# Kernel optimization log

Measured on AMD Instinct MI355X. Metric: run time of the kernel, lower is better.

Reference implementation:

```python
import jax, jax.numpy as jnp
import numpy as np

DIM = 768
NUM_HEADS = 12
HEAD_DIM = DIM // NUM_HEADS
SCALE = HEAD_DIM ** -0.5


def setup_inputs() -> dict:
    key = jax.random.key(0)
    k1, k2, k3, k4 = jax.random.split(key, 4)
    x = jax.random.normal(k1, (4, 2048, DIM), dtype=jnp.float32)
    # Linear weights stored as [in, out] (torch stores [out, in]; math identical)
    w_qkv = jax.random.normal(k2, (DIM, 3 * DIM), dtype=jnp.float32) * (DIM ** -0.5)
    w_proj = jax.random.normal(k3, (DIM, DIM), dtype=jnp.float32) * (DIM ** -0.5)
    b_proj = jax.random.normal(k4, (DIM,), dtype=jnp.float32) * 0.02
    return {"x": x, "w_qkv": w_qkv, "w_proj": w_proj, "b_proj": b_proj}


def reference(x, w_qkv, w_proj, b_proj):
    b, n, d = x.shape
    qkv = x @ w_qkv  # [b, n, 3*d]
    # '(qkv h d)' layout: leading split is qkv, then heads, then head_dim
    qkv = qkv.reshape(b, n, 3, NUM_HEADS, HEAD_DIM).transpose(2, 0, 3, 1, 4)
    q, k, v = qkv[0], qkv[1], qkv[2]  # each [b, h, n, hd]
    alpha = jnp.einsum('bhqd,bhkd->bhqk', q, k) * SCALE  # [b, h, n, n]
    attn = jax.nn.softmax(alpha, axis=-1)
    out = jnp.einsum('bhqk,bhkd->bhqd', attn, v)  # [b, h, n, hd]
    out = out.transpose(0, 2, 1, 3).reshape(b, n, d)  # b n (h d)
    return out @ w_proj + b_proj
```

## Files before the change

### kernel.cpp

```cpp
#include <hip/hip_runtime.h>
#include <hip/hip_bf16.h>


typedef short s16x8 __attribute__((ext_vector_type(8)));
typedef short s16x4 __attribute__((ext_vector_type(4)));
typedef float f32x4 __attribute__((ext_vector_type(4)));
typedef float f32x16 __attribute__((ext_vector_type(16)));
typedef unsigned int u32;
typedef unsigned int u32x2 __attribute__((ext_vector_type(2)));
typedef unsigned int u32x4 __attribute__((ext_vector_type(4)));

#define NHEADS 12
#define HDIM   64
#define SEQ    2048
#define BATCH  4
#define DMODEL 768
#define MTOT   (BATCH*SEQ)
#define K3     (3*DMODEL)
#define QSCALE 0.18033688f

#define CAST_BLOCKS ((MTOT * DMODEL / 4) / 256)
#define TQ_BLOCKS   ((K3 / 64) * (DMODEL / 64))
#define TP_BLOCKS   ((DMODEL / 64) * (DMODEL / 64))

__device__ __forceinline__ short f2bf(float f) {
  return __builtin_bit_cast(short, __float2bfloat16(f));
}
__device__ __forceinline__ u32 pack2bf_rh(float lo, float hi) {
  u32 a = __builtin_bit_cast(u32, lo) + 0x8000u;
  u32 b = __builtin_bit_cast(u32, hi) + 0x8000u;
  return __builtin_amdgcn_perm(b, a, 0x07060302u);
}
__device__ __forceinline__ u32 pack2bf_tr(float lo, float hi) {
  return __builtin_amdgcn_perm(__builtin_bit_cast(u32, hi),
                               __builtin_bit_cast(u32, lo), 0x07060302u);
}
__device__ __forceinline__ f32x4 mfma16(s16x8 a, s16x8 b, f32x4 c) {
  return __builtin_amdgcn_mfma_f32_16x16x32_bf16(a, b, c, 0, 0, 0);
}
__device__ __forceinline__ f32x16 mfma32(s16x8 a, s16x8 b, f32x16 c) {
  return __builtin_amdgcn_mfma_f32_32x32x16_bf16(a, b, c, 0, 0, 0);
}
__device__ __forceinline__ void gload_lds16(const void* g, void* l) {
  __builtin_amdgcn_global_load_lds(
      (const __attribute__((address_space(1))) void*)g,
      (__attribute__((address_space(3))) void*)l, 16, 0, 0);
}

__global__ __launch_bounds__(256) void k_prep(const float* __restrict__ x,
                                              const float* __restrict__ w_qkv,
                                              const float* __restrict__ w_proj,
                                              short* __restrict__ Xb,
                                              short* __restrict__ WqkvT,
                                              short* __restrict__ WprojT) {
  __shared__ short t[64][74];
  const int bid = blockIdx.x, tid = threadIdx.x;

  if (bid < CAST_BLOCKS) {
    int i = bid * 256 + tid;
    float4 f = reinterpret_cast<const float4*>(x)[i];
    s16x4 v;
    v[0] = f2bf(f.x); v[1] = f2bf(f.y); v[2] = f2bf(f.z); v[3] = f2bf(f.w);
    reinterpret_cast<s16x4*>(Xb)[i] = v;
    return;
  }
  const float* in;
  short* out;
  int C, idx;
  if (bid < CAST_BLOCKS + TQ_BLOCKS) {
    in = w_qkv; out = WqkvT; C = K3; idx = bid - CAST_BLOCKS;
  } else {
    in = w_proj; out = WprojT; C = DMODEL; idx = bid - CAST_BLOCKS - TQ_BLOCKS;
  }
  const int c0 = (idx % (C / 64)) * 64;
  const int r0 = (idx / (C / 64)) * 64;
  {
    const int r = tid >> 2, j0 = (tid & 3) * 16;
    const float* ip = in + (size_t)(r0 + r) * C + c0 + j0;
#pragma unroll
    for (int k = 0; k < 16; k += 4) {
      float4 f = *reinterpret_cast<const float4*>(ip + k);
      t[r][j0 + k + 0] = f2bf(f.x); t[r][j0 + k + 1] = f2bf(f.y);
      t[r][j0 + k + 2] = f2bf(f.z); t[r][j0 + k + 3] = f2bf(f.w);
    }
  }
  __syncthreads();
  {
    const int c = tid >> 2, rr0 = (tid & 3) * 16;
    short* op = out + (size_t)(c0 + c) * DMODEL + r0 + rr0;
#pragma unroll
    for (int k = 0; k < 16; k += 8) {
      s16x8 v;
#pragma unroll
      for (int q = 0; q < 8; ++q) v[q] = t[rr0 + k + q][c];
      *reinterpret_cast<s16x8*>(op + k) = v;
    }
  }
}

__global__ __launch_bounds__(512, 4) void k_gemm_qkv(const short* __restrict__ Xb,
                                                     const short* __restrict__ WT,
                                                     short* __restrict__ Qb,
                                                     short* __restrict__ Kb,
                                                     short* __restrict__ Vt) {
  __shared__ short As[2][128 * 64];
  __shared__ short Bs[2][128 * 64];
  const int tid = threadIdx.x;
  const int orig = blockIdx.y * gridDim.x + blockIdx.x;
  const int wg = (orig & 7) * (1152 / 8) + (orig >> 3);
  const int n0 = (wg % 18) * 128, m0 = (wg / 18) * 128;
  const int lane = tid & 63, w = tid >> 6;
  const int wr = w >> 2, wc = w & 3;
  const int g = lane >> 4, r16 = lane & 15;

  const int srow = tid >> 3;
  const int scc  = (tid & 7) ^ (srow & 7);
  const short* gaA = Xb + (size_t)(m0 + srow) * DMODEL + scc * 8;
  const short* gaB = WT + (size_t)(n0 + srow) * DMODEL + scc * 8;
  short* lA = &As[0][0] + w * 512;
  short* lB = &Bs[0][0] + w * 512;

#define GSTAGE(b, k0)                                                          \
  { gload_lds16(gaA + (k0),                         lA + (b) * 8192);          \
    gload_lds16(gaA + (size_t)64 * DMODEL + (k0),   lA + (b) * 8192 + 4096);   \
    gload_lds16(gaB + (k0),                         lB + (b) * 8192);          \
    gload_lds16(gaB + (size_t)64 * DMODEL + (k0),   lB + (b) * 8192 + 4096); }

  f32x4 acc[4][2] = {};
  const int key = (r16 & 7) << 4;

  GSTAGE(0, 0)
  for (int t = 0; t < DMODEL / 64; ++t) {
    const int b = t & 1;
    if (t + 1 < DMODEL / 64) {
      GSTAGE(b ^ 1, (t + 1) * 64)
      asm volatile("s_waitcnt vmcnt(4)" ::: "memory");
    } else {
      asm volatile("s_waitcnt vmcnt(0)" ::: "memory");
    }
    __builtin_amdgcn_s_barrier();
    __builtin_amdgcn_sched_barrier(0);

    const char* Ab = (const char*)&As[0][0] + b * 16384;
    const char* Bb = (const char*)&Bs[0][0] + b * 16384;
    s16x8 a[4][2], bf[2][2];
#pragma unroll
    for (int i = 0; i < 4; ++i)
#pragma unroll
      for (int kk = 0; kk < 2; ++kk)
        a[i][kk] = *(const s16x8*)(Ab + (((wr * 64 + i * 16 + r16) * 128 + kk * 64 + g * 16) ^ key));
#pragma unroll
    for (int j = 0; j < 2; ++j)
#pragma unroll
      for (int kk = 0; kk < 2; ++kk)
        bf[j][kk] = *(const s16x8*)(Bb + (((wc * 32 + j * 16 + r16) * 128 + kk * 64 + g * 16) ^ key));
#pragma unroll
    for (int kk = 0; kk < 2; ++kk)
#pragma unroll
      for (int i = 0; i < 4; ++i)
#pragma unroll
        for (int j = 0; j < 2; ++j)
          acc[i][j] = mfma16(a[i][kk], bf[j][kk], acc[i][j]);

    __builtin_amdgcn_sched_barrier(0);
    __builtin_amdgcn_s_barrier();
  }
#undef GSTAGE

#pragma unroll
  for (int i = 0; i < 4; ++i) {
#pragma unroll
    for (int jn = 0; jn < 2; ++jn) {
      const int c = n0 + wc * 32 + jn * 16 + r16;
#pragma unroll
      for (int rr = 0; rr < 4; ++rr) {
        const int m = m0 + wr * 64 + i * 16 + g * 4 + rr;
        const float a = acc[i][jn][rr];
        const int bb = m >> 11, ns = m & 2047;
        if (c < DMODEL) {
          const int h = c >> 6, d = c & 63;
          Qb[((bb * NHEADS + h) * SEQ + ns) * HDIM + d] = f2bf(a * QSCALE);
        } else if (c < 2 * DMODEL) {
          const int cc = c - DMODEL, h = cc >> 6, d = cc & 63;
          Kb[((bb * NHEADS + h) * SEQ + ns) * HDIM + d] = f2bf(a);
        } else {
          const int cc = c - 2 * DMODEL, h = cc >> 6, d = cc & 63;
          Vt[((bb * NHEADS + h) * HDIM + d) * SEQ + ns] = f2bf(a);
        }
      }
    }
  }
}

__global__ __launch_bounds__(256, 3) void k_attn(const short* __restrict__ Qb,
                                                 const short* __restrict__ Kb,
                                                 const short* __restrict__ Vtg,
                                                 short* __restrict__ Ctx) {
  __shared__ short Kt[2][64 * 64];
  __shared__ short Vt[2][64 * 64];

  const int tid = threadIdx.x, lane = tid & 63, w = tid >> 6;
  const int l31 = lane & 31, hi = lane >> 5;

  const int orig = blockIdx.y * gridDim.x + blockIdx.x;
  const int wg = (orig & 7) * (768 / 8) + (orig >> 3);
  const int qx = wg & 15;
  const int bh = wg >> 4;
  const int bb = bh / NHEADS, h = bh - bb * NHEADS;
  const int q0w = qx * 128 + w * 32;

  const short* Qp = Qb + (size_t)bh * SEQ * HDIM;
  const short* Kp = Kb + (size_t)bh * SEQ * HDIM;
  const short* Vp = Vtg + (size_t)bh * HDIM * SEQ;
  const int key4 = (lane & 7) << 4;

  const int sr1 = tid >> 3, sr2 = 32 + sr1;
  const int c1 = (tid & 7) ^ (sr1 & 7);
  const int c2 = (tid & 7) ^ (sr2 & 7);
  const short* kg1 = Kp + sr1 * HDIM + c1 * 8;
  const short* kg2 = Kp + sr2 * HDIM + c2 * 8;
  const short* vg1 = Vp + (size_t)sr1 * SEQ + c1 * 8;
  const short* vg2 = Vp + (size_t)sr2 * SEQ + c2 * 8;
  short* kld = &Kt[0][0] + w * 512;
  short* vld = &Vt[0][0] + w * 512;

#define STAGE(b, kb)                                                           \
  { gload_lds16(kg1 + (size_t)(kb) * HDIM, kld + (b) * 4096);                  \
    gload_lds16(kg2 + (size_t)(kb) * HDIM, kld + (b) * 4096 + 2048);           \
    gload_lds16(vg1 + (kb),                vld + (b) * 4096);                  \
    gload_lds16(vg2 + (kb),                vld + (b) * 4096 + 2048); }

  s16x8 aq[4];
#pragma unroll
  for (int kk = 0; kk < 4; ++kk)
    aq[kk] = *reinterpret_cast<const s16x8*>(&Qp[(q0w + l31) * HDIM + kk * 16 + hi * 8]);

  float sacc = 0.f;
  f32x16 accO[2] = {};

  STAGE(0, 0)

  for (int t = 0; t < SEQ / 64; ++t) {
    const int b = t & 1;
    if (t + 1 < SEQ / 64) {
      STAGE(b ^ 1, (t + 1) * 64)
      asm volatile("s_waitcnt vmcnt(4)" ::: "memory");
    } else {
      asm volatile("s_waitcnt vmcnt(0)" ::: "memory");
    }
    __builtin_amdgcn_s_barrier();
    __builtin_amdgcn_sched_barrier(0);

    const char* Kc = (const char*)Kt[b];
    const char* Vc = (const char*)Vt[b];

    f32x16 s0 = {}, s1 = {};
    __builtin_amdgcn_s_setprio(1);
#pragma unroll
    for (int kk = 0; kk < 4; ++kk) {
      const int cb = kk * 32 + hi * 16;
      s16x8 k0_ = *(const s16x8*)(Kc + (((l31)      * 128 + cb) ^ key4));
      s16x8 k1_ = *(const s16x8*)(Kc + (((l31 + 32) * 128 + cb) ^ key4));
      s0 = mfma32(k0_, aq[kk], s0);
      s1 = mfma32(k1_, aq[kk], s1);
    }
    __builtin_amdgcn_s_setprio(0);

    u32 A0[8], A1[8];
    float rs0 = 0.f, rs1 = 0.f, rs2 = 0.f, rs3 = 0.f;
#pragma unroll
    for (int r2 = 0; r2 < 8; ++r2) {
      float pa = __builtin_amdgcn_exp2f(s0[2 * r2]);
      float pb = __builtin_amdgcn_exp2f(s0[2 * r2 + 1]);
      rs0 += pa; rs1 += pb;
      A0[r2] = pack2bf_tr(pa, pb);
      float pc = __builtin_amdgcn_exp2f(s1[2 * r2]);
      float pd = __builtin_amdgcn_exp2f(s1[2 * r2 + 1]);
      rs2 += pc; rs3 += pd;
      A1[r2] = pack2bf_tr(pc, pd);
    }
    sacc += (rs0 + rs1) + (rs2 + rs3);

    __builtin_amdgcn_s_setprio(1);
#define PVW(Akg, KGOFF, S)                                                     \
    { u32 F0 = Akg[4 * (S)],     F2 = Akg[4 * (S) + 2];                        \
      u32 F1 = Akg[4 * (S) + 1], F3 = Akg[4 * (S) + 3];                        \
      asm volatile("v_permlane32_swap_b32 %0, %1" : "+v"(F0), "+v"(F2));       \
      asm volatile("v_permlane32_swap_b32 %0, %1" : "+v"(F1), "+v"(F3));       \
      u32x4 uv; uv[0] = F0; uv[1] = F1; uv[2] = F2; uv[3] = F3;                \
      s16x8 pfrag = __builtin_bit_cast(s16x8, uv);                             \
      const int cb_ = (KGOFF) + (S) * 32 + hi * 16;                            \
      s16x8 v0_ = *(const s16x8*)(Vc + (((l31)      * 128 + cb_) ^ key4));     \
      s16x8 v1_ = *(const s16x8*)(Vc + (((l31 + 32) * 128 + cb_) ^ key4));     \
      accO[0] = mfma32(v0_, pfrag, accO[0]);                                   \
      accO[1] = mfma32(v1_, pfrag, accO[1]); }
    PVW(A0, 0, 0) PVW(A0, 0, 1) PVW(A1, 64, 0) PVW(A1, 64, 1)
#undef PVW
    __builtin_amdgcn_s_setprio(0);

    __builtin_amdgcn_sched_barrier(0);
    __builtin_amdgcn_s_barrier();
  }
#undef STAGE

  sacc += __shfl_xor(sacc, 32);
  const float inv = 1.0f / sacc;
  short* rowp = Ctx + (size_t)(bb * SEQ + q0w + l31) * DMODEL + h * HDIM + 4 * hi;
#pragma unroll
  for (int dt = 0; dt < 2; ++dt) {
#pragma unroll
    for (int rq = 0; rq < 4; ++rq) {
      u32x2 ov;
      ov[0] = pack2bf_rh(accO[dt][rq * 4 + 0] * inv, accO[dt][rq * 4 + 1] * inv);
      ov[1] = pack2bf_rh(accO[dt][rq * 4 + 2] * inv, accO[dt][rq * 4 + 3] * inv);
      *reinterpret_cast<u32x2*>(rowp + dt * 32 + rq * 8) = ov;
    }
  }
}

__global__ __launch_bounds__(512, 4) void k_gemm_proj(const short* __restrict__ Ctx,
                                                      const short* __restrict__ WT,
                                                      const float* __restrict__ bias,
                                                      float* __restrict__ Out) {
  __shared__ short As[2][128 * 64];
  __shared__ short Bs[2][128 * 64];
  const int tid = threadIdx.x;
  const int orig = blockIdx.y * gridDim.x + blockIdx.x;
  const int wg = (orig & 7) * (384 / 8) + (orig >> 3);
  const int n0 = (wg % 6) * 128, m0 = (wg / 6) * 128;
  const int lane = tid & 63, w = tid >> 6;
  const int wr = w >> 2, wc = w & 3;
  const int g = lane >> 4, r16 = lane & 15;

  const int srow = tid >> 3;
  const int scc  = (tid & 7) ^ (srow & 7);
  const short* gaA = Ctx + (size_t)(m0 + srow) * DMODEL + scc * 8;
  const short* gaB = WT + (size_t)(n0 + srow) * DMODEL + scc * 8;
  short* lA = &As[0][0] + w * 512;
  short* lB = &Bs[0][0] + w * 512;

#define GSTAGE(b, k0)                                                          \
  { gload_lds16(gaA + (k0),                         lA + (b) * 8192);          \
    gload_lds16(gaA + (size_t)64 * DMODEL + (k0),   lA + (b) * 8192 + 4096);   \
    gload_lds16(gaB + (k0),                         lB + (b) * 8192);          \
    gload_lds16(gaB + (size_t)64 * DMODEL + (k0),   lB + (b) * 8192 + 4096); }

  f32x4 acc[4][2] = {};
  const int key = (r16 & 7) << 4;

  GSTAGE(0, 0)
  for (int t = 0; t < DMODEL / 64; ++t) {
    const int b = t & 1;
    if (t + 1 < DMODEL / 64) {
      GSTAGE(b ^ 1, (t + 1) * 64)
      asm volatile("s_waitcnt vmcnt(4)" ::: "memory");
    } else {
      asm volatile("s_waitcnt vmcnt(0)" ::: "memory");
    }
    __builtin_amdgcn_s_barrier();
    __builtin_amdgcn_sched_barrier(0);

    const char* Ab = (const char*)&As[0][0] + b * 16384;
    const char* Bb = (const char*)&Bs[0][0] + b * 16384;
    s16x8 a[4][2], bf[2][2];
#pragma unroll
    for (int i = 0; i < 4; ++i)
#pragma unroll
      for (int kk = 0; kk < 2; ++kk)
        a[i][kk] = *(const s16x8*)(Ab + (((wr * 64 + i * 16 + r16) * 128 + kk * 64 + g * 16) ^ key));
#pragma unroll
    for (int j = 0; j < 2; ++j)
#pragma unroll
      for (int kk = 0; kk < 2; ++kk)
        bf[j][kk] = *(const s16x8*)(Bb + (((wc * 32 + j * 16 + r16) * 128 + kk * 64 + g * 16) ^ key));
#pragma unroll
    for (int kk = 0; kk < 2; ++kk)
#pragma unroll
      for (int i = 0; i < 4; ++i)
#pragma unroll
        for (int j = 0; j < 2; ++j)
          acc[i][j] = mfma16(a[i][kk], bf[j][kk], acc[i][j]);

    __builtin_amdgcn_sched_barrier(0);
    __builtin_amdgcn_s_barrier();
  }
#undef GSTAGE

#pragma unroll
  for (int i = 0; i < 4; ++i) {
#pragma unroll
    for (int jn = 0; jn < 2; ++jn) {
      const int c = n0 + wc * 32 + jn * 16 + r16;
      const float bv = bias[c];
#pragma unroll
      for (int rr = 0; rr < 4; ++rr) {
        const int m = m0 + wr * 64 + i * 16 + g * 4 + rr;
        Out[(size_t)m * DMODEL + c] = acc[i][jn][rr] + bv;
      }
    }
  }
}

extern "C" void kernel_launch(void* const* d_in, const int* in_sizes, int n_in,
                              void* d_out, int out_size, void* d_ws, size_t ws_size,
                              hipStream_t stream) {
  const float* x      = (const float*)d_in[0];
  const float* w_qkv  = (const float*)d_in[1];
  const float* w_proj = (const float*)d_in[2];
  const float* b_proj = (const float*)d_in[3];
  float* out = (float*)d_out;

  char* ws = (char*)d_ws;
  const size_t SZ_X = (size_t)MTOT * DMODEL * 2;
  short* Xb     = (short*)ws;                 ws += SZ_X;
  short* WqkvT  = (short*)ws;                 ws += (size_t)K3 * DMODEL * 2;
  short* WprojT = (short*)ws;                 ws += (size_t)DMODEL * DMODEL * 2;
  short* Qb     = (short*)ws;                 ws += SZ_X;
  short* Kb     = (short*)ws;                 ws += SZ_X;
  short* Vt     = (short*)ws;                 ws += SZ_X;
  short* Ctxb   = Xb;

  k_prep<<<CAST_BLOCKS + TQ_BLOCKS + TP_BLOCKS, 256, 0, stream>>>(
      x, w_qkv, w_proj, Xb, WqkvT, WprojT);

  k_gemm_qkv<<<dim3(K3 / 128, MTOT / 128), 512, 0, stream>>>(Xb, WqkvT, Qb, Kb, Vt);
  k_attn<<<dim3(SEQ / 128, BATCH * NHEADS), 256, 0, stream>>>(Qb, Kb, Vt, Ctxb);
  k_gemm_proj<<<dim3(DMODEL / 128, MTOT / 128), 512, 0, stream>>>(Ctxb, WprojT, b_proj, out);
}
```

Baseline: 155.6 us.

## Double attention key tile to 128 and interleave softmax with PV MFMAs

The attention kernel now stages 128 keys per iteration instead of 64. The K and V LDS buffers are doubled, the loop count is halved, and launch bounds drop from 3 to 2 blocks per CU to fit the larger shared memory. The exp/pack work for the two halves of the tile is split so the PV MFMAs for the first half can overlap the softmax of the second. This halves the number of barriers and global-load issue points per key, at the cost of occupancy and more register pressure from four score accumulators.

```diff
diff --git a/kernel.cpp b/kernel.cpp
--- a/kernel.cpp
+++ b/kernel.cpp
@@ -192,12 +192,12 @@
   }
 }
 
-__global__ __launch_bounds__(256, 3) void k_attn(const short* __restrict__ Qb,
+__global__ __launch_bounds__(256, 2) void k_attn(const short* __restrict__ Qb,
                                                  const short* __restrict__ Kb,
                                                  const short* __restrict__ Vtg,
                                                  short* __restrict__ Ctx) {
-  __shared__ short Kt[2][64 * 64];
-  __shared__ short Vt[2][64 * 64];
+  __shared__ short Kt[2][128 * 64];
+  __shared__ short Vt[2][64 * 128];
 
   const int tid = threadIdx.x, lane = tid & 63, w = tid >> 6;
   const int l31 = lane & 31, hi = lane >> 5;
@@ -214,37 +214,41 @@
   const short* Vp = Vtg + (size_t)bh * HDIM * SEQ;
   const int key4 = (lane & 7) << 4;
 
-  const int sr1 = tid >> 3, sr2 = 32 + sr1;
-  const int c1 = (tid & 7) ^ (sr1 & 7);
-  const int c2 = (tid & 7) ^ (sr2 & 7);
-  const short* kg1 = Kp + sr1 * HDIM + c1 * 8;
-  const short* kg2 = Kp + sr2 * HDIM + c2 * 8;
-  const short* vg1 = Vp + (size_t)sr1 * SEQ + c1 * 8;
-  const short* vg2 = Vp + (size_t)sr2 * SEQ + c2 * 8;
+  const int krow = tid >> 3;
+  const int kch  = (tid & 7) ^ (krow & 7);
+  const short* kg = Kp + krow * HDIM + kch * 8;
+  const int vrow = tid >> 4;
+  const int vch  = (tid & 15) ^ (vrow & 7);
+  const short* vg = Vp + (size_t)vrow * SEQ + vch * 8;
   short* kld = &Kt[0][0] + w * 512;
   short* vld = &Vt[0][0] + w * 512;
 
 #define STAGE(b, kb)                                                           \
-  { gload_lds16(kg1 + (size_t)(kb) * HDIM, kld + (b) * 4096);                  \
-    gload_lds16(kg2 + (size_t)(kb) * HDIM, kld + (b) * 4096 + 2048);           \
-    gload_lds16(vg1 + (kb),                vld + (b) * 4096);                  \
-    gload_lds16(vg2 + (kb),                vld + (b) * 4096 + 2048); }
+  { gload_lds16(kg + (size_t)((kb))      * HDIM, kld + (b) * 8192);            \
+    gload_lds16(kg + (size_t)((kb) + 32) * HDIM, kld + (b) * 8192 + 2048);     \
+    gload_lds16(kg + (size_t)((kb) + 64) * HDIM, kld + (b) * 8192 + 4096);     \
+    gload_lds16(kg + (size_t)((kb) + 96) * HDIM, kld + (b) * 8192 + 6144);     \
+    gload_lds16(vg + (kb),                       vld + (b) * 8192);            \
+    gload_lds16(vg + (size_t)16 * SEQ + (kb),    vld + (b) * 8192 + 2048);     \
+    gload_lds16(vg + (size_t)32 * SEQ + (kb),    vld + (b) * 8192 + 4096);     \
+    gload_lds16(vg + (size_t)48 * SEQ + (kb),    vld + (b) * 8192 + 6144); }
 
   s16x8 aq[4];
 #pragma unroll
   for (int kk = 0; kk < 4; ++kk)
     aq[kk] = *reinterpret_cast<const s16x8*>(&Qp[(q0w + l31) * HDIM + kk * 16 + hi * 8]);
 
+  const f32x16 Z = {};
   float sacc = 0.f;
   f32x16 accO[2] = {};
 
   STAGE(0, 0)
 
-  for (int t = 0; t < SEQ / 64; ++t) {
+  for (int t = 0; t < SEQ / 128; ++t) {
     const int b = t & 1;
-    if (t + 1 < SEQ / 64) {
-      STAGE(b ^ 1, (t + 1) * 64)
-      asm volatile("s_waitcnt vmcnt(4)" ::: "memory");
+    if (t + 1 < SEQ / 128) {
+      STAGE(b ^ 1, (t + 1) * 128)
+      asm volatile("s_waitcnt vmcnt(8)" ::: "memory");
     } else {
       asm volatile("s_waitcnt vmcnt(0)" ::: "memory");
     }
@@ -254,34 +258,27 @@
     const char* Kc = (const char*)Kt[b];
     const char* Vc = (const char*)Vt[b];
 
-    f32x16 s0 = {}, s1 = {};
+#define KLD(R, CB) (*(const s16x8*)(Kc + (((l31 + (R)) * 128 + (CB)) ^ key4)))
+    f32x16 s0, s1, s2, s3;
     __builtin_amdgcn_s_setprio(1);
-#pragma unroll
-    for (int kk = 0; kk < 4; ++kk) {
+    {
+      const int cb = hi * 16;
+      s0 = mfma32(KLD(0, cb),  aq[0], Z);
+      s1 = mfma32(KLD(32, cb), aq[0], Z);
+      s2 = mfma32(KLD(64, cb), aq[0], Z);
+      s3 = mfma32(KLD(96, cb), aq[0], Z);
+    }
+#pragma unroll
+    for (int kk = 1; kk < 4; ++kk) {
       const int cb = kk * 32 + hi * 16;
-      s16x8 k0_ = *(const s16x8*)(Kc + (((l31)      * 128 + cb) ^ key4));
-      s16x8 k1_ = *(const s16x8*)(Kc + (((l31 + 32) * 128 + cb) ^ key4));
-      s0 = mfma32(k0_, aq[kk], s0);
-      s1 = mfma32(k1_, aq[kk], s1);
-    }
+      s0 = mfma32(KLD(0, cb),  aq[kk], s0);
+      s1 = mfma32(KLD(32, cb), aq[kk], s1);
+      s2 = mfma32(KLD(64, cb), aq[kk], s2);
+      s3 = mfma32(KLD(96, cb), aq[kk], s3);
+    }
+#undef KLD
     __builtin_amdgcn_s_setprio(0);
 
-    u32 A0[8], A1[8];
-    float rs0 = 0.f, rs1 = 0.f, rs2 = 0.f, rs3 = 0.f;
-#pragma unroll
-    for (int r2 = 0; r2 < 8; ++r2) {
-      float pa = __builtin_amdgcn_exp2f(s0[2 * r2]);
-      float pb = __builtin_amdgcn_exp2f(s0[2 * r2 + 1]);
-      rs0 += pa; rs1 += pb;
-      A0[r2] = pack2bf_tr(pa, pb);
-      float pc = __builtin_amdgcn_exp2f(s1[2 * r2]);
-      float pd = __builtin_amdgcn_exp2f(s1[2 * r2 + 1]);
-      rs2 += pc; rs3 += pd;
-      A1[r2] = pack2bf_tr(pc, pd);
-    }
-    sacc += (rs0 + rs1) + (rs2 + rs3);
-
-    __builtin_amdgcn_s_setprio(1);
 #define PVW(Akg, KGOFF, S)                                                     \
     { u32 F0 = Akg[4 * (S)],     F2 = Akg[4 * (S) + 2];                        \
       u32 F1 = Akg[4 * (S) + 1], F3 = Akg[4 * (S) + 3];                        \
@@ -290,13 +287,49 @@
       u32x4 uv; uv[0] = F0; uv[1] = F1; uv[2] = F2; uv[3] = F3;                \
       s16x8 pfrag = __builtin_bit_cast(s16x8, uv);                             \
       const int cb_ = (KGOFF) + (S) * 32 + hi * 16;                            \
-      s16x8 v0_ = *(const s16x8*)(Vc + (((l31)      * 128 + cb_) ^ key4));     \
-      s16x8 v1_ = *(const s16x8*)(Vc + (((l31 + 32) * 128 + cb_) ^ key4));     \
+      s16x8 v0_ = *(const s16x8*)(Vc + (((l31)      * 256 + cb_) ^ key4));     \
+      s16x8 v1_ = *(const s16x8*)(Vc + (((l31 + 32) * 256 + cb_) ^ key4));     \
       accO[0] = mfma32(v0_, pfrag, accO[0]);                                   \
       accO[1] = mfma32(v1_, pfrag, accO[1]); }
-    PVW(A0, 0, 0) PVW(A0, 0, 1) PVW(A1, 64, 0) PVW(A1, 64, 1)
+
+    float rs0 = 0.f, rs1 = 0.f;
+    {
+      u32 A0[8], A1[8];
+#pragma unroll
+      for (int r2 = 0; r2 < 8; ++r2) {
+        float pa = __builtin_amdgcn_exp2f(s0[2 * r2]);
+        float pb = __builtin_amdgcn_exp2f(s0[2 * r2 + 1]);
+        rs0 += pa + pb;
+        A0[r2] = pack2bf_tr(pa, pb);
+        float pc = __builtin_amdgcn_exp2f(s1[2 * r2]);
+        float pd = __builtin_amdgcn_exp2f(s1[2 * r2 + 1]);
+        rs1 += pc + pd;
+        A1[r2] = pack2bf_tr(pc, pd);
+      }
+      __builtin_amdgcn_s_setprio(1);
+      PVW(A0, 0, 0) PVW(A0, 0, 1) PVW(A1, 64, 0) PVW(A1, 64, 1)
+      __builtin_amdgcn_s_setprio(0);
+    }
+    float rs2 = 0.f, rs3 = 0.f;
+    {
+      u32 A2[8], A3[8];
+#pragma unroll
+      for (int r2 = 0; r2 < 8; ++r2) {
+        float pa = __builtin_amdgcn_exp2f(s2[2 * r2]);
+        float pb = __builtin_amdgcn_exp2f(s2[2 * r2 + 1]);
+        rs2 += pa + pb;
+        A2[r2] = pack2bf_tr(pa, pb);
+        float pc = __builtin_amdgcn_exp2f(s3[2 * r2]);
+        float pd = __builtin_amdgcn_exp2f(s3[2 * r2 + 1]);
+        rs3 += pc + pd;
+        A3[r2] = pack2bf_tr(pc, pd);
+      }
+      __builtin_amdgcn_s_setprio(1);
+      PVW(A2, 128, 0) PVW(A2, 128, 1) PVW(A3, 192, 0) PVW(A3, 192, 1)
+      __builtin_amdgcn_s_setprio(0);
+    }
 #undef PVW
-    __builtin_amdgcn_s_setprio(0);
+    sacc += (rs0 + rs1) + (rs2 + rs3);
 
     __builtin_amdgcn_sched_barrier(0);
     __builtin_amdgcn_s_barrier();
```

Result: slower. 159.2 us (+2.3%).
